# Kernel optimization log

Measured on AMD Instinct MI355X. Metric: run time of the kernel, lower is better.

## Reference

```python
import jax, jax.numpy as jnp
import numpy as np

E, F, T, C = 158, 2049, 64, 2  # embed dim, freq bins, time frames, num sources
B = 8


def setup_inputs() -> dict:
    key = jax.random.key(0)
    k1, k2, k3, k4 = jax.random.split(key, 4)
    xs = jax.random.normal(k1, (B, E, F, T), dtype=jnp.float32)
    x_indicator = jax.random.normal(k2, (B, C), dtype=jnp.float32)
    # torch.nn.Linear(C, E*F): weight [E*F, C], bias [E*F]
    W = jax.random.normal(k3, (E * F, C), dtype=jnp.float32) * (1.0 / np.sqrt(C))
    b = jax.random.normal(k4, (E * F,), dtype=jnp.float32) * 0.01
    return {"xs": xs, "x_indicator": x_indicator, "W": W, "b": b}


def reference(xs, x_indicator, W, b):
    # proj = Linear(indicator): [B, E*F]
    proj = x_indicator @ W.T + b
    # torch .view(T, F*E) on contiguous [E,F,T] == row-major reshape to [T, E*F]
    Xv = xs.reshape(B, T, E * F)
    # Rx[b, t] = <Xv[b, t, :], proj[b, :]>  (shape [B, T])
    Rx = jnp.einsum('btk,bk->bt', Xv, proj)
    # rank-1 outer product per sample: [B, E*F, T]
    obs = proj[:, :, None] * Rx[:, None, :]
    # elementwise gate on the input embedding
    out = xs * obs.reshape(B, E, F, T)
    # indicator_projection.view(-1, F, E) per sample -> [B, F, E]
    anchor = proj.reshape(B, F, E)
    return out, anchor
```

## Files before the change

### kernel.cpp

```cpp
#include <hip/hip_runtime.h>

#define E_ 158
#define F_ 2049
#define T_ 64
#define C_ 2
#define B_ 8
#define EF 323742
#define EF2 161871
#define EFT 20719488
#define NOUT 165755904
#define N4TOT 41438976
#define NSEG 16
#define SEG2 10117

__global__ __launch_bounds__(256) void proj_kernel(
    const float* __restrict__ xind, const float* __restrict__ W,
    const float* __restrict__ bias, float* __restrict__ anchor)
{
    unsigned int idx = blockIdx.x * 256u + threadIdx.x;
    if (idx >= (unsigned int)(B_ * EF)) return;
    unsigned int b = idx / (unsigned int)EF;
    unsigned int k = idx - b * (unsigned int)EF;
    anchor[idx] = xind[b * 2 + 0] * W[2 * k + 0]
                + xind[b * 2 + 1] * W[2 * k + 1]
                + bias[k];
}

__global__ __launch_bounds__(256) void rx_all_kernel(
    const float* __restrict__ xs, const float* __restrict__ proj,
    float* __restrict__ part)
{
    const int blk = blockIdx.x;
    const int b = blk >> 10;
    const int t = (blk >> 4) & 63;
    const int s = blk & 15;
    const int len2 = (s == NSEG - 1) ? (EF2 - (NSEG - 1) * SEG2) : SEG2;

    const float2* __restrict__ xp =
        (const float2*)(xs + (size_t)b * EFT) + (size_t)t * EF2 + (size_t)s * SEG2;
    const float2* __restrict__ pp =
        (const float2*)(proj + (size_t)b * EF) + (size_t)s * SEG2;

    float acc = 0.f;
    #pragma unroll 4
    for (int i = threadIdx.x; i < len2; i += 256) {
        float2 x = xp[i];
        float2 p = pp[i];
        acc += x.x * p.x + x.y * p.y;
    }
    #pragma unroll
    for (int off = 32; off > 0; off >>= 1)
        acc += __shfl_down(acc, off, 64);

    __shared__ float sacc[4];
    if ((threadIdx.x & 63) == 0) sacc[threadIdx.x >> 6] = acc;
    __syncthreads();
    if (threadIdx.x == 0)
        part[blk] = sacc[0] + sacc[1] + sacc[2] + sacc[3];
}

__global__ __launch_bounds__(512) void rx_final_kernel(
    const float* __restrict__ part, float* __restrict__ Rx)
{
    const int bt = threadIdx.x;
    float r = 0.f;
    #pragma unroll
    for (int s = 0; s < NSEG; ++s) r += part[bt * NSEG + s];
    Rx[bt] = r;
}

__global__ __launch_bounds__(256) void gate_all_kernel(
    const float* __restrict__ xs, const float* __restrict__ proj,
    const float* __restrict__ Rx, float* __restrict__ out)
{
    unsigned int rb = (unsigned int)(gridDim.x - 1u - blockIdx.x);
    unsigned int idx4 = rb * 256u + threadIdx.x;
    unsigned int i = idx4 * 4u;
    unsigned int b = i / (unsigned int)EFT;
    unsigned int r = i - b * (unsigned int)EFT;
    unsigned int k = r >> 6;
    unsigned int t = r & 63u;

    float p = proj[(size_t)b * EF + k];
    const float4 rx4 = *(const float4*)(Rx + b * T_ + t);
    float4 x = ((const float4*)xs)[idx4];
    float4 o;
    o.x = x.x * p * rx4.x;
    o.y = x.y * p * rx4.y;
    o.z = x.z * p * rx4.z;
    o.w = x.w * p * rx4.w;
    ((float4*)out)[idx4] = o;
}

extern "C" void kernel_launch(void* const* d_in, const int* in_sizes, int n_in,
                              void* d_out, int out_size, void* d_ws, size_t ws_size,
                              hipStream_t stream)
{
    const float* xs   = (const float*)d_in[0];
    const float* xind = (const float*)d_in[1];
    const float* W    = (const float*)d_in[2];
    const float* bias = (const float*)d_in[3];

    float* out    = (float*)d_out;
    float* anchor = (float*)d_out + (size_t)NOUT;
    float* part   = (float*)d_ws;
    float* Rx     = (float*)d_ws + B_ * T_ * NSEG;

    {
        const int n = B_ * EF;
        proj_kernel<<<(n + 255) / 256, 256, 0, stream>>>(xind, W, bias, anchor);
    }
    rx_all_kernel<<<B_ * T_ * NSEG, 256, 0, stream>>>(xs, anchor, part);
    rx_final_kernel<<<1, 512, 0, stream>>>(part, Rx);
    gate_all_kernel<<<N4TOT / 256, 256, 0, stream>>>(xs, anchor, Rx, out);
}
```

Before: 369.7 us.

## Stage proj segments in LDS for reuse across time frames; nontemporal gate I/O

The Rx reduction now launches one block per (segment, batch). Each block loads its proj slice into shared memory once, and each wavefront then reduces 16 time frames against that slice, so proj is no longer re-read from global memory for every frame. This cuts the block count from 8192 to 960 and raises the partial-sum segment count to 120, which makes the final reduction longer. The gate kernel also switches to nontemporal vector loads and stores so the streaming xs/out traffic bypasses cache retention.

```diff
diff --git a/kernel.cpp b/kernel.cpp
--- a/kernel.cpp
+++ b/kernel.cpp
@@ -10,8 +10,12 @@
 #define EFT 20719488
 #define NOUT 165755904
 #define N4TOT 41438976
-#define NSEG 16
-#define SEG2 10117
+
+#define NSEG 120
+#define SEGF2 1349
+#define LASTF2 1340
+
+typedef float vfloat4 __attribute__((ext_vector_type(4)));
 
 __global__ __launch_bounds__(256) void proj_kernel(
     const float* __restrict__ xind, const float* __restrict__ W,
@@ -30,33 +34,40 @@
     const float* __restrict__ xs, const float* __restrict__ proj,
     float* __restrict__ part)
 {
-    const int blk = blockIdx.x;
-    const int b = blk >> 10;
-    const int t = (blk >> 4) & 63;
-    const int s = blk & 15;
-    const int len2 = (s == NSEG - 1) ? (EF2 - (NSEG - 1) * SEG2) : SEG2;
+    const int s = blockIdx.x;
+    const int b = blockIdx.y;
+    const int len = (s == NSEG - 1) ? LASTF2 : SEGF2;
 
-    const float2* __restrict__ xp =
-        (const float2*)(xs + (size_t)b * EFT) + (size_t)t * EF2 + (size_t)s * SEG2;
-    const float2* __restrict__ pp =
-        (const float2*)(proj + (size_t)b * EF) + (size_t)s * SEG2;
+    __shared__ float2 sproj[SEGF2];
+    {
+        const float2* __restrict__ pp =
+            (const float2*)proj + (size_t)b * EF2 + (size_t)s * SEGF2;
+        for (int i = threadIdx.x; i < len; i += 256)
+            sproj[i] = pp[i];
+    }
+    __syncthreads();
 
-    float acc = 0.f;
-    #pragma unroll 4
-    for (int i = threadIdx.x; i < len2; i += 256) {
-        float2 x = xp[i];
-        float2 p = pp[i];
-        acc += x.x * p.x + x.y * p.y;
+    const int w = threadIdx.x >> 6;
+    const int lane = threadIdx.x & 63;
+    const float2* __restrict__ xb =
+        (const float2*)xs + (size_t)b * (EFT / 2) + (size_t)s * SEGF2;
+
+    #pragma unroll 2
+    for (int j = 0; j < 16; ++j) {
+        const int t = w * 16 + j;
+        const float2* __restrict__ xp = xb + (size_t)t * EF2;
+        float acc = 0.f;
+        for (int i = lane; i < len; i += 64) {
+            float2 x = xp[i];
+            float2 p = sproj[i];
+            acc += x.x * p.x + x.y * p.y;
+        }
+        #pragma unroll
+        for (int off = 32; off > 0; off >>= 1)
+            acc += __shfl_down(acc, off, 64);
+        if (lane == 0)
+            part[(size_t)(b * 64 + t) * NSEG + s] = acc;
     }
-    #pragma unroll
-    for (int off = 32; off > 0; off >>= 1)
-        acc += __shfl_down(acc, off, 64);
-
-    __shared__ float sacc[4];
-    if ((threadIdx.x & 63) == 0) sacc[threadIdx.x >> 6] = acc;
-    __syncthreads();
-    if (threadIdx.x == 0)
-        part[blk] = sacc[0] + sacc[1] + sacc[2] + sacc[3];
 }
 
 __global__ __launch_bounds__(512) void rx_final_kernel(
@@ -64,7 +75,6 @@
 {
     const int bt = threadIdx.x;
     float r = 0.f;
-    #pragma unroll
     for (int s = 0; s < NSEG; ++s) r += part[bt * NSEG + s];
     Rx[bt] = r;
 }
@@ -83,13 +93,13 @@
 
     float p = proj[(size_t)b * EF + k];
     const float4 rx4 = *(const float4*)(Rx + b * T_ + t);
-    float4 x = ((const float4*)xs)[idx4];
-    float4 o;
+    vfloat4 x = __builtin_nontemporal_load(&((const vfloat4*)xs)[idx4]);
+    vfloat4 o;
     o.x = x.x * p * rx4.x;
     o.y = x.y * p * rx4.y;
     o.z = x.z * p * rx4.z;
     o.w = x.w * p * rx4.w;
-    ((float4*)out)[idx4] = o;
+    __builtin_nontemporal_store(o, &((vfloat4*)out)[idx4]);
 }
 
 extern "C" void kernel_launch(void* const* d_in, const int* in_sizes, int n_in,
@@ -104,13 +114,13 @@
     float* out    = (float*)d_out;
     float* anchor = (float*)d_out + (size_t)NOUT;
     float* part   = (float*)d_ws;
-    float* Rx     = (float*)d_ws + B_ * T_ * NSEG;
+    float* Rx     = (float*)d_ws + 512 * NSEG;
 
     {
         const int n = B_ * EF;
         proj_kernel<<<(n + 255) / 256, 256, 0, stream>>>(xind, W, bias, anchor);
     }
-    rx_all_kernel<<<B_ * T_ * NSEG, 256, 0, stream>>>(xs, anchor, part);
+    rx_all_kernel<<<dim3(NSEG, B_), 256, 0, stream>>>(xs, anchor, part);
     rx_final_kernel<<<1, 512, 0, stream>>>(part, Rx);
     gate_all_kernel<<<N4TOT / 256, 256, 0, stream>>>(xs, anchor, Rx, out);
 }
```

New measurement: 417.5 us. 1.13x slower.
